# Performance work log

Measured on AMD Instinct MI355X. Metric: run time of the kernel, lower is better.

Reference implementation:

```python
import jax, jax.numpy as jnp
import numpy as np

B = 2048        # batch
D_DENSE = 13    # dense input features
F = 7           # number of sparse features
CARD = 10000    # cardinality per sparse feature (== len(tokenizer_values))
E = 64          # embedding dim per feature
D_OUT = 32      # dense arch output size
S_OUT = 32      # sparse arch output size per feature
D_HID = 2 * D_OUT   # DenseArch MLP hidden (output_size*2 per code)
S_HID = 2 * S_OUT   # SparseArch MLP hidden (output_size*2 per code)
CONCAT = D_OUT + F * S_OUT    # 256
P_IN = CONCAT * CONCAT        # 65536, flattened outer product
P_HID = 512


def setup_inputs() -> dict:
    key = jax.random.key(0)
    ks = jax.random.split(key, 18)
    s = 0.05
    return {
        "dense_features": jax.random.normal(ks[0], (B, D_DENSE), dtype=jnp.float32),
        "sparse_features": jax.random.randint(ks[1], (B, F), 0, CARD, dtype=jnp.int64),
        # tokenizer_values per feature (shared arange, as in metadata)
        "tokenizers": jnp.arange(CARD, dtype=jnp.int64),
        # embedding tables stacked over features: [F, CARD, E]
        "emb_tables": jax.random.normal(ks[2], (F, CARD, E), dtype=jnp.float32) * s,
        # DenseArch MLP
        "dw1": jax.random.normal(ks[3], (D_DENSE, D_HID), dtype=jnp.float32) * s,
        "db1": jnp.zeros((D_HID,), dtype=jnp.float32),
        "dw2": jax.random.normal(ks[4], (D_HID, D_OUT), dtype=jnp.float32) * s,
        "db2": jnp.zeros((D_OUT,), dtype=jnp.float32),
        # per-feature sparse MLPs stacked over features
        "sw1": jax.random.normal(ks[5], (F, E, S_HID), dtype=jnp.float32) * s,
        "sb1": jnp.zeros((F, S_HID), dtype=jnp.float32),
        "sw2": jax.random.normal(ks[6], (F, S_HID, S_OUT), dtype=jnp.float32) * s,
        "sb2": jnp.zeros((F, S_OUT), dtype=jnp.float32),
        # PredictionLayer MLP
        "pw1": jax.random.normal(ks[7], (P_IN, P_HID), dtype=jnp.float32) * s,
        "pb1": jnp.zeros((P_HID,), dtype=jnp.float32),
        "pw2": jax.random.normal(ks[8], (P_HID, 1), dtype=jnp.float32) * s,
        "pb2": jnp.zeros((1,), dtype=jnp.float32),
    }


def reference(dense_features, sparse_features, tokenizers, emb_tables,
              dw1, db1, dw2, db2, sw1, sb1, sw2, sb2, pw1, pb1, pw2, pb2):
    # DenseArch: MLP(13 -> 64 -> 32)
    dense_out = jnp.maximum(dense_features @ dw1 + db1, 0.0) @ dw2 + db2  # [B, D_OUT]

    # SparseArch: equality-match argmax indexing (faithful to get_indices),
    # then embedding gather and per-feature MLP, vectorized over features.
    matches = sparse_features[:, :, None] == tokenizers[None, None, :]  # [B, F, CARD]
    idx = jnp.argmax(matches, axis=2)                                   # [B, F]
    gathered = emb_tables[jnp.arange(emb_tables.shape[0])[None, :], idx]  # [B, F, E]
    h = jnp.maximum(jnp.einsum('bfe,feh->bfh', gathered, sw1) + sb1, 0.0)
    sparse_out = jnp.einsum('bfh,fho->bfo', h, sw2) + sb2                # [B, F, S_OUT]

    # DenseSparseInteractionLayer: concat -> outer product -> flatten
    concat = jnp.concatenate(
        [dense_out, sparse_out.reshape(sparse_out.shape[0], -1)], axis=1)  # [B, CONCAT]
    outer = jnp.einsum('bi,bj->bij', concat, concat)
    flattened = outer.reshape(concat.shape[0], -1)                       # [B, CONCAT^2]

    # PredictionLayer: MLP(CONCAT^2 -> P_HID -> 1) + sigmoid, squeeze
    logits = jnp.maximum(flattened @ pw1 + pb1, 0.0) @ pw2 + pb2
    return jax.nn.sigmoid(logits).squeeze()
```

## Files before the change

kernel.cpp:

```cpp
#include <hip/hip_runtime.h>
#include <hip/hip_fp16.h>
#include <math.h>

#define BATCH 2048
#define NFEAT 7
#define CARD 10000
#define CONCAT 256
#define P_HID 512

#define BM 128
#define BN 128
#define BK 64
#define KSPLIT 16
#define NUNITS 640
#define TILES_PER_SPLIT 40
#define UNIT_ST (512 * 64)

using f16x4   = __attribute__((ext_vector_type(4))) _Float16;
using half8   = __attribute__((ext_vector_type(8))) _Float16;
using floatx4 = __attribute__((ext_vector_type(4))) float;

__device__ __forceinline__ void dma16(const _Float16* g, _Float16* l) {
    __builtin_amdgcn_global_load_lds(
        (const __attribute__((address_space(1))) unsigned int*)g,
        (__attribute__((address_space(3))) unsigned int*)l,
        16, 0, 0);
}

__device__ __forceinline__ void unit_decode(int u, int& i, int& jw) {
    if (u < 256)      { i = u;                jw = u >> 6; }
    else if (u < 448) { int v = u - 256; i = v / 3;        jw = 1 + v % 3; }
    else if (u < 576) { int v = u - 448; i = 64 + (v >> 1); jw = 2 + (v & 1); }
    else              { i = 128 + (u - 576); jw = 3; }
}

__global__ __launch_bounds__(256) void fused_pre(
    const float* __restrict__ dense, const int* __restrict__ sparse,
    const float* __restrict__ emb,
    const float* __restrict__ dw1, const float* __restrict__ db1,
    const float* __restrict__ dw2, const float* __restrict__ db2,
    const float* __restrict__ sw1, const float* __restrict__ sb1,
    const float* __restrict__ sw2, const float* __restrict__ sb2,
    const float* __restrict__ pw1,
    _Float16* __restrict__ cbf, _Float16* __restrict__ St)
{
    __shared__ __align__(16) _Float16 sh[64 * 256];
    const int tid = threadIdx.x;

    if (blockIdx.x < NUNITS) {
        const int u = blockIdx.x;
        int i, jw;
        unit_decode(u, i, jw);

        for (int nh = 0; nh < 2; ++nh) {
            const int nb = nh * 256;
            if (nh) __syncthreads();

#pragma unroll
            for (int m = 0; m < 16; ++m) {
                const int flat = m * 256 + tid;
                const int q = flat >> 6, c4 = flat & 63;
                const int j = (jw << 6) + q;
                float4 s = {0.f, 0.f, 0.f, 0.f};
                if (j >= i) {
                    s = *(const float4*)(pw1 + ((size_t)i * 256 + j) * P_HID + nb + 4 * c4);
                    if (j > i) {
                        const float4 mv = *(const float4*)(pw1 + ((size_t)j * 256 + i) * P_HID + nb + 4 * c4);
                        s.x += mv.x; s.y += mv.y; s.z += mv.z; s.w += mv.w;
                    }
                }
                f16x4 hv = {(_Float16)s.x, (_Float16)s.y, (_Float16)s.z, (_Float16)s.w};
                *(f16x4*)(sh + q * 256 + 4 * c4) = hv;
            }
            __syncthreads();

            const _Float16* col = sh + tid;
            _Float16* outp = St + (size_t)u * UNIT_ST + (size_t)(nb + tid) * 64;
#pragma unroll
            for (int e = 0; e < 8; ++e) {
                half8 o;
#pragma unroll
                for (int r = 0; r < 8; ++r) o[r] = col[(8 * e + r) * 256];
                *(half8*)(outp + 8 * e) = o;
            }
        }
    } else {
        float* smem = (float*)sh;
        const int wv = tid >> 6, t = tid & 63;
        const int b = (blockIdx.x - NUNITS) * 4 + wv;
        float* xs   = smem + wv * 13;
        float* bufA = smem + 64  + wv * 64;
        float* bufB = smem + 320 + wv * 64;

        if (t < 13) xs[t] = dense[b * 13 + t];
        __syncthreads();

        float h = db1[t];
#pragma unroll
        for (int d = 0; d < 13; ++d) h += xs[d] * dw1[d * 64 + t];
        bufA[t] = fmaxf(h, 0.f);
        __syncthreads();

        if (t < 32) {
            float o = db2[t];
#pragma unroll
            for (int k = 0; k < 64; ++k) o += bufA[k] * dw2[k * 32 + t];
            cbf[b * 256 + t] = (_Float16)o;
        }

        for (int f = 0; f < NFEAT; ++f) {
            __syncthreads();
            const int idx = sparse[b * NFEAT + f];
            bufB[t] = emb[((size_t)(f * CARD + idx)) * 64 + t];
            __syncthreads();
            float s = sb1[f * 64 + t];
#pragma unroll
            for (int e = 0; e < 64; ++e) s += bufB[e] * sw1[(f * 64 + e) * 64 + t];
            bufA[t] = fmaxf(s, 0.f);
            __syncthreads();
            if (t < 32) {
                float o = sb2[f * 32 + t];
#pragma unroll
                for (int k = 0; k < 64; ++k) o += bufA[k] * sw2[(f * 64 + k) * 32 + t];
                cbf[b * 256 + 32 + f * 32 + t] = (_Float16)o;
            }
        }
    }
}

__global__ __launch_bounds__(256, 4) void bilinear_gemm(
    const _Float16* __restrict__ cbf, const _Float16* __restrict__ St,
    _Float16* __restrict__ hidpart)
{
    __shared__ _Float16 Al[BM][BK + 8];
    __shared__ _Float16 Bl[BN][BK];

    const int b = blockIdx.x;
    const int xcd = b & 7, slot = b >> 3;
    const int mt = slot & 15;
    const int slice = ((slot >> 4) << 3) | xcd;
    const int nt = slice & 3, ks = slice >> 2;
    const int m0 = mt * BM, n0 = nt * BN;
    const int t0 = ks * TILES_PER_SPLIT;

    const int tid = threadIdx.x, lane = tid & 63, wv = tid >> 6;
    const int wrow = (wv & 1) * 64, wcol = (wv >> 1) * 64;
    const int arow = tid >> 1, ajoff = (tid & 1) * 32;

    floatx4 acc[4][4];
#pragma unroll
    for (int i = 0; i < 4; ++i)
#pragma unroll
        for (int j = 0; j < 4; ++j) acc[i][j] = (floatx4){0.f, 0.f, 0.f, 0.f};

    const _Float16* crow = cbf + (m0 + arow) * 256;
    const int drow = wv * 32 + (lane >> 3);
    const int eswz = (lane & 7) ^ ((lane >> 3) & 7);
    const _Float16* bsrc = St + (size_t)t0 * UNIT_ST + (size_t)(n0 + drow) * 64 + eswz * 8;
    _Float16* bdst = &Bl[wv * 32][0];

    for (int it = 0; it < TILES_PER_SPLIT; ++it) {
#pragma unroll
        for (int p = 0; p < 4; ++p)
            dma16(bsrc + (size_t)(p * 8) * 64, bdst + (p * 8) * BK);
        bsrc += UNIT_ST;

        int ui, ujw;
        unit_decode(t0 + it, ui, ujw);
        const _Float16 ci = crow[ui];
        const half8 civ = {ci, ci, ci, ci, ci, ci, ci, ci};
        const _Float16* cj = crow + (ujw << 6) + ajoff;
#pragma unroll
        for (int x = 0; x < 32; x += 8) {
            half8 v = *(const half8*)(cj + x);
            *(half8*)&Al[arow][ajoff + x] = v * civ;
        }
        __syncthreads();

#pragma unroll
        for (int kk = 0; kk < BK; kk += 32) {
            half8 af[4], bfr[4];
#pragma unroll
            for (int i = 0; i < 4; ++i)
                af[i] = *(const half8*)&Al[wrow + i * 16 + (lane & 15)][kk + (lane >> 4) * 8];
#pragma unroll
            for (int j = 0; j < 4; ++j) {
                const int s = (((kk >> 3) + (lane >> 4)) ^ (lane & 7)) * 8;
                bfr[j] = *(const half8*)&Bl[wcol + j * 16 + (lane & 15)][s];
            }
#pragma unroll
            for (int i = 0; i < 4; ++i)
#pragma unroll
                for (int j = 0; j < 4; ++j)
                    acc[i][j] = __builtin_amdgcn_mfma_f32_16x16x32_f16(
                        af[i], bfr[j], acc[i][j], 0, 0, 0);
        }
        __syncthreads();
    }

    _Float16* outp = hidpart + (size_t)ks * BATCH * P_HID;
    const int r0 = m0 + wrow + (lane >> 4) * 4;
    const int c0 = n0 + wcol + (lane & 15);
#pragma unroll
    for (int i = 0; i < 4; ++i)
#pragma unroll
        for (int j = 0; j < 4; ++j)
#pragma unroll
            for (int r = 0; r < 4; ++r)
                outp[(size_t)(r0 + i * 16 + r) * P_HID + c0 + j * 16] =
                    (_Float16)acc[i][j][r];
}

__global__ __launch_bounds__(256) void finalize(
    const _Float16* __restrict__ hidpart,
    const float* __restrict__ pb1,
    const float* __restrict__ pw2,
    const float* __restrict__ pb2,
    float* __restrict__ out)
{
    const int b = blockIdx.x, t = threadIdx.x;
    const int wv = t >> 6, lane = t & 63;

    float acc[8];
#pragma unroll
    for (int k = 0; k < 8; ++k) acc[k] = 0.f;

#pragma unroll
    for (int si = 0; si < 4; ++si) {
        const int s = wv + 4 * si;
        const half8 v = *(const half8*)(hidpart + (size_t)s * BATCH * P_HID
                                        + (size_t)b * P_HID + lane * 8);
#pragma unroll
        for (int k = 0; k < 8; ++k) acc[k] += (float)v[k];
    }

    __shared__ float red[4 * 512];
#pragma unroll
    for (int k = 0; k < 8; ++k) red[wv * 512 + k * 64 + lane] = acc[k];
    __syncthreads();

    if (wv == 0) {
        float dot = 0.f;
#pragma unroll
        for (int k = 0; k < 8; ++k) {
            const int n = lane * 8 + k;
            float v = red[k * 64 + lane] + red[512 + k * 64 + lane]
                    + red[1024 + k * 64 + lane] + red[1536 + k * 64 + lane];
            v += pb1[n];
            v = fmaxf(v, 0.f);
            dot += v * pw2[n];
        }
#pragma unroll
        for (int off = 32; off; off >>= 1) dot += __shfl_down(dot, off, 64);
        if (lane == 0) {
            const float s = dot + pb2[0];
            out[b] = 1.f / (1.f + expf(-s));
        }
    }
}

extern "C" void kernel_launch(void* const* d_in, const int* in_sizes, int n_in,
                              void* d_out, int out_size, void* d_ws, size_t ws_size,
                              hipStream_t stream)
{
    const float* dense  = (const float*)d_in[0];
    const int*   sparse = (const int*)d_in[1];
    const float* emb = (const float*)d_in[3];
    const float* dw1 = (const float*)d_in[4];
    const float* db1 = (const float*)d_in[5];
    const float* dw2 = (const float*)d_in[6];
    const float* db2 = (const float*)d_in[7];
    const float* sw1 = (const float*)d_in[8];
    const float* sb1 = (const float*)d_in[9];
    const float* sw2 = (const float*)d_in[10];
    const float* sb2 = (const float*)d_in[11];
    const float* pw1 = (const float*)d_in[12];
    const float* pb1 = (const float*)d_in[13];
    const float* pw2 = (const float*)d_in[14];
    const float* pb2 = (const float*)d_in[15];

    char* ws = (char*)d_ws;
    _Float16* cbf     = (_Float16*)ws;
    _Float16* St      = (_Float16*)(ws + (1 << 20));
    _Float16* hidpart = (_Float16*)(ws + (1 << 20) + ((size_t)40 << 20));

    fused_pre<<<NUNITS + BATCH / 4, 256, 0, stream>>>(
        dense, sparse, emb, dw1, db1, dw2, db2, sw1, sb1, sw2, sb2, pw1,
        cbf, St);
    bilinear_gemm<<<16 * 4 * KSPLIT, 256, 0, stream>>>(cbf, St, hidpart);
    finalize<<<BATCH, 256, 0, stream>>>(hidpart, pb1, pw2, pb2, (float*)d_out);
}
```

Before: 360.3 us.

## Double-buffer B tiles, build A fragments in registers, split prep blocks

The bilinear GEMM now double-buffers the B tile in LDS so the next tile's DMA is issued while the current one is consumed, and it drops one __syncthreads per iteration. The A operand (the c_i*c_j outer-product slice) is loaded directly from global memory into MFMA fragment registers instead of being staged through LDS. Separately, the weight-folding prep kernel splits each unit across two blocks (one per half of N) and uses nontemporal loads for pw1. Together these aim to hide memory latency and raise prep parallelism, at the cost of more LDS for B, more registers, and redundant global loads of A rows across waves. The single barrier per iteration relies on that barrier to order both buffer reuse and DMA completion.

```diff
diff --git a/kernel.cpp b/kernel.cpp
--- a/kernel.cpp
+++ b/kernel.cpp
@@ -15,6 +15,7 @@
 #define NUNITS 640
 #define TILES_PER_SPLIT 40
 #define UNIT_ST (512 * 64)
+#define PREP_BLOCKS (NUNITS * 2)
 
 using f16x4   = __attribute__((ext_vector_type(4))) _Float16;
 using half8   = __attribute__((ext_vector_type(8))) _Float16;
@@ -47,47 +48,45 @@
     __shared__ __align__(16) _Float16 sh[64 * 256];
     const int tid = threadIdx.x;
 
-    if (blockIdx.x < NUNITS) {
-        const int u = blockIdx.x;
+    if (blockIdx.x < PREP_BLOCKS) {
+        const int u = blockIdx.x >> 1, nh = blockIdx.x & 1;
+        const int nb = nh * 256;
         int i, jw;
         unit_decode(u, i, jw);
 
-        for (int nh = 0; nh < 2; ++nh) {
-            const int nb = nh * 256;
-            if (nh) __syncthreads();
-
-#pragma unroll
-            for (int m = 0; m < 16; ++m) {
-                const int flat = m * 256 + tid;
-                const int q = flat >> 6, c4 = flat & 63;
-                const int j = (jw << 6) + q;
-                float4 s = {0.f, 0.f, 0.f, 0.f};
-                if (j >= i) {
-                    s = *(const float4*)(pw1 + ((size_t)i * 256 + j) * P_HID + nb + 4 * c4);
-                    if (j > i) {
-                        const float4 mv = *(const float4*)(pw1 + ((size_t)j * 256 + i) * P_HID + nb + 4 * c4);
-                        s.x += mv.x; s.y += mv.y; s.z += mv.z; s.w += mv.w;
-                    }
+#pragma unroll
+        for (int m = 0; m < 16; ++m) {
+            const int flat = m * 256 + tid;
+            const int q = flat >> 6, c4 = flat & 63;
+            const int j = (jw << 6) + q;
+            floatx4 s = {0.f, 0.f, 0.f, 0.f};
+            if (j >= i) {
+                s = __builtin_nontemporal_load(
+                    (const floatx4*)(pw1 + ((size_t)i * 256 + j) * P_HID + nb + 4 * c4));
+                if (j > i) {
+                    const floatx4 mv = __builtin_nontemporal_load(
+                        (const floatx4*)(pw1 + ((size_t)j * 256 + i) * P_HID + nb + 4 * c4));
+                    s += mv;
                 }
-                f16x4 hv = {(_Float16)s.x, (_Float16)s.y, (_Float16)s.z, (_Float16)s.w};
-                *(f16x4*)(sh + q * 256 + 4 * c4) = hv;
             }
-            __syncthreads();
-
-            const _Float16* col = sh + tid;
-            _Float16* outp = St + (size_t)u * UNIT_ST + (size_t)(nb + tid) * 64;
-#pragma unroll
-            for (int e = 0; e < 8; ++e) {
-                half8 o;
-#pragma unroll
-                for (int r = 0; r < 8; ++r) o[r] = col[(8 * e + r) * 256];
-                *(half8*)(outp + 8 * e) = o;
-            }
+            f16x4 hv = {(_Float16)s.x, (_Float16)s.y, (_Float16)s.z, (_Float16)s.w};
+            *(f16x4*)(sh + q * 256 + 4 * c4) = hv;
+        }
+        __syncthreads();
+
+        const _Float16* col = sh + tid;
+        _Float16* outp = St + (size_t)u * UNIT_ST + (size_t)(nb + tid) * 64;
+#pragma unroll
+        for (int e = 0; e < 8; ++e) {
+            half8 o;
+#pragma unroll
+            for (int r = 0; r < 8; ++r) o[r] = col[(8 * e + r) * 256];
+            *(half8*)(outp + 8 * e) = o;
         }
     } else {
         float* smem = (float*)sh;
         const int wv = tid >> 6, t = tid & 63;
-        const int b = (blockIdx.x - NUNITS) * 4 + wv;
+        const int b = (blockIdx.x - PREP_BLOCKS) * 4 + wv;
         float* xs   = smem + wv * 13;
         float* bufA = smem + 64  + wv * 64;
         float* bufB = smem + 320 + wv * 64;
@@ -132,8 +131,7 @@
     const _Float16* __restrict__ cbf, const _Float16* __restrict__ St,
     _Float16* __restrict__ hidpart)
 {
-    __shared__ _Float16 Al[BM][BK + 8];
-    __shared__ _Float16 Bl[BN][BK];
+    __shared__ _Float16 Bl[2][BN][BK];
 
     const int b = blockIdx.x;
     const int xcd = b & 7, slot = b >> 3;
@@ -145,7 +143,8 @@
 
     const int tid = threadIdx.x, lane = tid & 63, wv = tid >> 6;
     const int wrow = (wv & 1) * 64, wcol = (wv >> 1) * 64;
-    const int arow = tid >> 1, ajoff = (tid & 1) * 32;
+    const int l15 = lane & 15, l4 = lane >> 4, l7 = lane & 7;
+    const int koff = l4 * 8;
 
     floatx4 acc[4][4];
 #pragma unroll
@@ -153,54 +152,72 @@
 #pragma unroll
         for (int j = 0; j < 4; ++j) acc[i][j] = (floatx4){0.f, 0.f, 0.f, 0.f};
 
-    const _Float16* crow = cbf + (m0 + arow) * 256;
+    const _Float16* rowp[4];
+#pragma unroll
+    for (int i = 0; i < 4; ++i)
+        rowp[i] = cbf + (size_t)(m0 + wrow + i * 16 + l15) * 256;
+
     const int drow = wv * 32 + (lane >> 3);
     const int eswz = (lane & 7) ^ ((lane >> 3) & 7);
     const _Float16* bsrc = St + (size_t)t0 * UNIT_ST + (size_t)(n0 + drow) * 64 + eswz * 8;
-    _Float16* bdst = &Bl[wv * 32][0];
+
+#pragma unroll
+    for (int p = 0; p < 4; ++p)
+        dma16(bsrc + (size_t)(p * 8) * 64, &Bl[0][wv * 32 + p * 8][0]);
+    bsrc += UNIT_ST;
 
     for (int it = 0; it < TILES_PER_SPLIT; ++it) {
-#pragma unroll
-        for (int p = 0; p < 4; ++p)
-            dma16(bsrc + (size_t)(p * 8) * 64, bdst + (p * 8) * BK);
-        bsrc += UNIT_ST;
-
+        const int cur = it & 1;
         int ui, ujw;
         unit_decode(t0 + it, ui, ujw);
-        const _Float16 ci = crow[ui];
-        const half8 civ = {ci, ci, ci, ci, ci, ci, ci, ci};
-        const _Float16* cj = crow + (ujw << 6) + ajoff;
-#pragma unroll
-        for (int x = 0; x < 32; x += 8) {
-            half8 v = *(const half8*)(cj + x);
-            *(half8*)&Al[arow][ajoff + x] = v * civ;
-        }
+
+        half8 w0[4], w1[4];
+        _Float16 ci[4];
+#pragma unroll
+        for (int i = 0; i < 4; ++i) {
+            const _Float16* rp = rowp[i];
+            ci[i] = rp[ui];
+            const _Float16* wb = rp + (ujw << 6) + koff;
+            w0[i] = *(const half8*)(wb);
+            w1[i] = *(const half8*)(wb + 32);
+        }
+
         __syncthreads();
 
-#pragma unroll
-        for (int kk = 0; kk < BK; kk += 32) {
-            half8 af[4], bfr[4];
-#pragma unroll
-            for (int i = 0; i < 4; ++i)
-                af[i] = *(const half8*)&Al[wrow + i * 16 + (lane & 15)][kk + (lane >> 4) * 8];
-#pragma unroll
-            for (int j = 0; j < 4; ++j) {
-                const int s = (((kk >> 3) + (lane >> 4)) ^ (lane & 7)) * 8;
-                bfr[j] = *(const half8*)&Bl[wcol + j * 16 + (lane & 15)][s];
-            }
+        if (it + 1 < TILES_PER_SPLIT) {
+#pragma unroll
+            for (int p = 0; p < 4; ++p)
+                dma16(bsrc + (size_t)(p * 8) * 64, &Bl[cur ^ 1][wv * 32 + p * 8][0]);
+            bsrc += UNIT_ST;
+        }
+
+#pragma unroll
+        for (int i = 0; i < 4; ++i) {
+            const half8 civ = {ci[i], ci[i], ci[i], ci[i], ci[i], ci[i], ci[i], ci[i]};
+            w0[i] *= civ;
+            w1[i] *= civ;
+        }
+
+#pragma unroll
+        for (int h = 0; h < 2; ++h) {
+            const int kk = h * 32;
+            const int s = (((kk >> 3) + l4) ^ l7) * 8;
+            half8 bfr[4];
+#pragma unroll
+            for (int j = 0; j < 4; ++j)
+                bfr[j] = *(const half8*)&Bl[cur][wcol + j * 16 + l15][s];
 #pragma unroll
             for (int i = 0; i < 4; ++i)
 #pragma unroll
                 for (int j = 0; j < 4; ++j)
                     acc[i][j] = __builtin_amdgcn_mfma_f32_16x16x32_f16(
-                        af[i], bfr[j], acc[i][j], 0, 0, 0);
-        }
-        __syncthreads();
+                        h ? w1[i] : w0[i], bfr[j], acc[i][j], 0, 0, 0);
+        }
     }
 
     _Float16* outp = hidpart + (size_t)ks * BATCH * P_HID;
-    const int r0 = m0 + wrow + (lane >> 4) * 4;
-    const int c0 = n0 + wcol + (lane & 15);
+    const int r0 = m0 + wrow + l4 * 4;
+    const int c0 = n0 + wcol + l15;
 #pragma unroll
     for (int i = 0; i < 4; ++i)
 #pragma unroll
@@ -284,7 +301,7 @@
     _Float16* St      = (_Float16*)(ws + (1 << 20));
     _Float16* hidpart = (_Float16*)(ws + (1 << 20) + ((size_t)40 << 20));
 
-    fused_pre<<<NUNITS + BATCH / 4, 256, 0, stream>>>(
+    fused_pre<<<PREP_BLOCKS + BATCH / 4, 256, 0, stream>>>(
         dense, sparse, emb, dw1, db1, dw2, db2, sw1, sb1, sw2, sb2, pw1,
         cbf, St);
     bilinear_gemm<<<16 * 4 * KSPLIT, 256, 0, stream>>>(cbf, St, hidpart);
```

New measurement: 529.2 us. +46.9%, slower.

## Rebalance split-K to 12 uneven splits, split prep blocks, preload A row chunks

Applied to the files above, without the earlier changes.

The prep kernel now gives each half of the hidden dimension its own block, doubling the block count, and reads the 128MB fp32 weight with nontemporal loads. The bilinear GEMM drops from 16 to 12 K-splits of 53 or 54 tiles, giving 768 blocks. That fits roughly one wave at the lowered occupancy bound of 3 blocks per CU, and finalize has fewer partials to sum. The A operand's row chunks are loaded into registers once and the next tile's scalar is prefetched, which removes per-tile global loads but raises register pressure.

```diff
diff --git a/kernel.cpp b/kernel.cpp
--- a/kernel.cpp
+++ b/kernel.cpp
@@ -11,10 +11,10 @@
 #define BM 128
 #define BN 128
 #define BK 64
-#define KSPLIT 16
+#define KSPLIT 12
 #define NUNITS 640
-#define TILES_PER_SPLIT 40
 #define UNIT_ST (512 * 64)
+#define PREP_BLOCKS (NUNITS * 2)
 
 using f16x4   = __attribute__((ext_vector_type(4))) _Float16;
 using half8   = __attribute__((ext_vector_type(8))) _Float16;
@@ -33,6 +33,9 @@
     else if (u < 576) { int v = u - 448; i = 64 + (v >> 1); jw = 2 + (v & 1); }
     else              { i = 128 + (u - 576); jw = 3; }
 }
+
+__device__ __forceinline__ int split_t0(int ks)     { return ks * 53 + (ks < 4 ? ks : 4); }
+__device__ __forceinline__ int split_ntiles(int ks) { return 53 + (ks < 4 ? 1 : 0); }
 
 __global__ __launch_bounds__(256) void fused_pre(
     const float* __restrict__ dense, const int* __restrict__ sparse,
@@ -47,47 +50,45 @@
     __shared__ __align__(16) _Float16 sh[64 * 256];
     const int tid = threadIdx.x;
 
-    if (blockIdx.x < NUNITS) {
-        const int u = blockIdx.x;
+    if (blockIdx.x < PREP_BLOCKS) {
+        const int u = blockIdx.x >> 1, nh = blockIdx.x & 1;
+        const int nb = nh * 256;
         int i, jw;
         unit_decode(u, i, jw);
 
-        for (int nh = 0; nh < 2; ++nh) {
-            const int nb = nh * 256;
-            if (nh) __syncthreads();
-
-#pragma unroll
-            for (int m = 0; m < 16; ++m) {
-                const int flat = m * 256 + tid;
-                const int q = flat >> 6, c4 = flat & 63;
-                const int j = (jw << 6) + q;
-                float4 s = {0.f, 0.f, 0.f, 0.f};
-                if (j >= i) {
-                    s = *(const float4*)(pw1 + ((size_t)i * 256 + j) * P_HID + nb + 4 * c4);
-                    if (j > i) {
-                        const float4 mv = *(const float4*)(pw1 + ((size_t)j * 256 + i) * P_HID + nb + 4 * c4);
-                        s.x += mv.x; s.y += mv.y; s.z += mv.z; s.w += mv.w;
-                    }
+#pragma unroll
+        for (int m = 0; m < 16; ++m) {
+            const int flat = m * 256 + tid;
+            const int q = flat >> 6, c4 = flat & 63;
+            const int j = (jw << 6) + q;
+            floatx4 s = {0.f, 0.f, 0.f, 0.f};
+            if (j >= i) {
+                s = __builtin_nontemporal_load(
+                    (const floatx4*)(pw1 + ((size_t)i * 256 + j) * P_HID + nb + 4 * c4));
+                if (j > i) {
+                    const floatx4 mv = __builtin_nontemporal_load(
+                        (const floatx4*)(pw1 + ((size_t)j * 256 + i) * P_HID + nb + 4 * c4));
+                    s += mv;
                 }
-                f16x4 hv = {(_Float16)s.x, (_Float16)s.y, (_Float16)s.z, (_Float16)s.w};
-                *(f16x4*)(sh + q * 256 + 4 * c4) = hv;
             }
-            __syncthreads();
-
-            const _Float16* col = sh + tid;
-            _Float16* outp = St + (size_t)u * UNIT_ST + (size_t)(nb + tid) * 64;
-#pragma unroll
-            for (int e = 0; e < 8; ++e) {
-                half8 o;
-#pragma unroll
-                for (int r = 0; r < 8; ++r) o[r] = col[(8 * e + r) * 256];
-                *(half8*)(outp + 8 * e) = o;
-            }
+            f16x4 hv = {(_Float16)s.x, (_Float16)s.y, (_Float16)s.z, (_Float16)s.w};
+            *(f16x4*)(sh + q * 256 + 4 * c4) = hv;
+        }
+        __syncthreads();
+
+        const _Float16* col = sh + tid;
+        _Float16* outp = St + (size_t)u * UNIT_ST + (size_t)(nb + tid) * 64;
+#pragma unroll
+        for (int e = 0; e < 8; ++e) {
+            half8 o;
+#pragma unroll
+            for (int r = 0; r < 8; ++r) o[r] = col[(8 * e + r) * 256];
+            *(half8*)(outp + 8 * e) = o;
         }
     } else {
         float* smem = (float*)sh;
         const int wv = tid >> 6, t = tid & 63;
-        const int b = (blockIdx.x - NUNITS) * 4 + wv;
+        const int b = (blockIdx.x - PREP_BLOCKS) * 4 + wv;
         float* xs   = smem + wv * 13;
         float* bufA = smem + 64  + wv * 64;
         float* bufB = smem + 320 + wv * 64;
@@ -128,7 +129,7 @@
     }
 }
 
-__global__ __launch_bounds__(256, 4) void bilinear_gemm(
+__global__ __launch_bounds__(256, 3) void bilinear_gemm(
     const _Float16* __restrict__ cbf, const _Float16* __restrict__ St,
     _Float16* __restrict__ hidpart)
 {
@@ -141,7 +142,8 @@
     const int slice = ((slot >> 4) << 3) | xcd;
     const int nt = slice & 3, ks = slice >> 2;
     const int m0 = mt * BM, n0 = nt * BN;
-    const int t0 = ks * TILES_PER_SPLIT;
+    const int t0 = split_t0(ks);
+    const int ntiles = split_ntiles(ks);
 
     const int tid = threadIdx.x, lane = tid & 63, wv = tid >> 6;
     const int wrow = (wv & 1) * 64, wcol = (wv >> 1) * 64;
@@ -154,28 +156,51 @@
         for (int j = 0; j < 4; ++j) acc[i][j] = (floatx4){0.f, 0.f, 0.f, 0.f};
 
     const _Float16* crow = cbf + (m0 + arow) * 256;
+
+    half8 pre[4][4];
+#pragma unroll
+    for (int jw = 0; jw < 4; ++jw)
+#pragma unroll
+        for (int x = 0; x < 4; ++x)
+            pre[jw][x] = *(const half8*)(crow + (jw << 6) + ajoff + 8 * x);
+
     const int drow = wv * 32 + (lane >> 3);
     const int eswz = (lane & 7) ^ ((lane >> 3) & 7);
     const _Float16* bsrc = St + (size_t)t0 * UNIT_ST + (size_t)(n0 + drow) * 64 + eswz * 8;
     _Float16* bdst = &Bl[wv * 32][0];
 
-    for (int it = 0; it < TILES_PER_SPLIT; ++it) {
+    int ui_c, ujw_c;
+    unit_decode(t0, ui_c, ujw_c);
+    _Float16 ci_c = crow[ui_c];
+
+    for (int it = 0; it < ntiles; ++it) {
 #pragma unroll
         for (int p = 0; p < 4; ++p)
             dma16(bsrc + (size_t)(p * 8) * 64, bdst + (p * 8) * BK);
         bsrc += UNIT_ST;
 
-        int ui, ujw;
-        unit_decode(t0 + it, ui, ujw);
-        const _Float16 ci = crow[ui];
-        const half8 civ = {ci, ci, ci, ci, ci, ci, ci, ci};
-        const _Float16* cj = crow + (ujw << 6) + ajoff;
-#pragma unroll
-        for (int x = 0; x < 32; x += 8) {
-            half8 v = *(const half8*)(cj + x);
-            *(half8*)&Al[arow][ajoff + x] = v * civ;
-        }
-        __syncthreads();
+        {
+            const half8 civ = {ci_c, ci_c, ci_c, ci_c, ci_c, ci_c, ci_c, ci_c};
+            _Float16* dst = &Al[arow][ajoff];
+#define AGEN(JW)                                                         \
+            { *(half8*)(dst +  0) = pre[JW][0] * civ;                    \
+              *(half8*)(dst +  8) = pre[JW][1] * civ;                    \
+              *(half8*)(dst + 16) = pre[JW][2] * civ;                    \
+              *(half8*)(dst + 24) = pre[JW][3] * civ; }
+            switch (ujw_c) {
+                case 0:  AGEN(0); break;
+                case 1:  AGEN(1); break;
+                case 2:  AGEN(2); break;
+                default: AGEN(3); break;
+            }
+#undef AGEN
+        }
+        __syncthreads();
+
+        if (it + 1 < ntiles) {
+            unit_decode(t0 + it + 1, ui_c, ujw_c);
+            ci_c = crow[ui_c];
+        }
 
 #pragma unroll
         for (int kk = 0; kk < BK; kk += 32) {
@@ -226,7 +251,7 @@
     for (int k = 0; k < 8; ++k) acc[k] = 0.f;
 
 #pragma unroll
-    for (int si = 0; si < 4; ++si) {
+    for (int si = 0; si < 3; ++si) {
         const int s = wv + 4 * si;
         const half8 v = *(const half8*)(hidpart + (size_t)s * BATCH * P_HID
                                         + (size_t)b * P_HID + lane * 8);
@@ -284,7 +309,7 @@
     _Float16* St      = (_Float16*)(ws + (1 << 20));
     _Float16* hidpart = (_Float16*)(ws + (1 << 20) + ((size_t)40 << 20));
 
-    fused_pre<<<NUNITS + BATCH / 4, 256, 0, stream>>>(
+    fused_pre<<<PREP_BLOCKS + BATCH / 4, 256, 0, stream>>>(
         dense, sparse, emb, dw1, db1, dw2, db2, sw1, sb1, sw2, sb2, pw1,
         cbf, St);
     bilinear_gemm<<<16 * 4 * KSPLIT, 256, 0, stream>>>(cbf, St, hidpart);
```

Result: faster. 349.3 us (-3.1%).
